# Kernel tuning notes

Measured on AMD Instinct MI355X. Metric: run time of the kernel, lower is better.

## Reference

```python
import jax, jax.numpy as jnp
import numpy as np

CUR, FULL, BS, DIM, H, D = 512, 1024, 4, 1024, 16, 64
PREV = FULL - CUR


def _rel_shift(x):
    # x: (cur, full, bs, h) -- TransformerXL relative shift (pad/reshape/slice)
    cur, full = x.shape[0], x.shape[1]
    zero_pad = jnp.zeros((cur, 1) + x.shape[2:], x.dtype)
    x_padded = jnp.concatenate([zero_pad, x], axis=1)           # (cur, full+1, bs, h)
    x_padded = x_padded.reshape((full + 1, cur) + x.shape[2:])  # view trick
    x = x_padded[1:].reshape(x.shape)
    tri = jnp.tril(jnp.ones((cur, full), x.dtype), full - cur)  # keep valid band
    return x * tri[:, :, None, None]


def setup_inputs() -> dict:
    key = jax.random.key(0)
    ks = jax.random.split(key, 12)
    s = jnp.float32(0.02)
    # causal mask: query i (at absolute pos i+PREV) may not attend to key j > i+PREV
    mask = (jnp.arange(FULL)[None, :] > (jnp.arange(CUR)[:, None] + PREV))[:, :, None]
    return {
        "inputs": jax.random.normal(ks[0], (CUR, BS, DIM), jnp.float32),
        "pos_embedding": jax.random.normal(ks[1], (FULL, 1, DIM), jnp.float32),
        "full_input": jax.random.normal(ks[2], (FULL, BS, DIM), jnp.float32),
        "u": jax.random.normal(ks[3], (H, D), jnp.float32) * s,
        "v": jax.random.normal(ks[4], (H, D), jnp.float32) * s,
        "W_kv": jax.random.normal(ks[5], (DIM, 2 * H * D), jnp.float32) * s,
        "b_kv": jnp.zeros((2 * H * D,), jnp.float32),
        "W_q": jax.random.normal(ks[6], (DIM, H * D), jnp.float32) * s,
        "b_q": jnp.zeros((H * D,), jnp.float32),
        "W_pos": jax.random.normal(ks[7], (DIM, H * D), jnp.float32) * s,
        "b_pos": jnp.zeros((H * D,), jnp.float32),
        "W_proj": jax.random.normal(ks[8], (H * D, DIM), jnp.float32) * s,
        "b_proj": jnp.zeros((DIM,), jnp.float32),
        "mask": mask,
    }


def reference(inputs, pos_embedding, full_input, u, v, W_kv, b_kv, W_q, b_q,
              W_pos, b_pos, W_proj, b_proj, mask):
    cur_seq, bs = inputs.shape[0], inputs.shape[1]
    full_seq = full_input.shape[0]
    scale = jnp.float32(1.0 / D ** 0.5)

    kv = full_input @ W_kv + b_kv                       # (full, bs, 2*H*D)
    key, value = jnp.split(kv, 2, axis=-1)
    query = inputs @ W_q + b_q                          # (cur, bs, H*D)
    r = (pos_embedding @ W_pos + b_pos).reshape(full_seq, H, D)

    key = key.reshape(full_seq, bs, H, D)
    value = value.reshape(full_seq, bs, H, D)
    query = query.reshape(cur_seq, bs, H, D)

    content_attn = jnp.einsum('ibhd,jbhd->ijbh', query + u, key)
    position_attn = jnp.einsum('ibhd,jhd->ijbh', query + v, r)
    position_attn = _rel_shift(position_attn)

    attn = (content_attn + position_attn) * scale       # (cur, full, bs, h)
    attn = jnp.where(mask[:, :, :, None], -jnp.inf, attn)
    attn = jax.nn.softmax(attn, axis=1)                 # softmax over full_seq

    attn_vec = jnp.einsum('ijbh,jbhd->ibhd', attn, value)
    attn_vec = attn_vec.reshape(cur_seq, bs, H * D)
    return attn_vec @ W_proj + b_proj                   # (cur, bs, DIM)
```

## Files before the change

### kernel.cpp

```cpp
#include <hip/hip_runtime.h>


typedef unsigned short u16;
typedef short short8 __attribute__((ext_vector_type(8)));
typedef float f32x4 __attribute__((ext_vector_type(4)));

#define BSZ 4
#define PREV 512

__device__ __forceinline__ float b2f(u16 u) {
  union { unsigned int i; float f; } x; x.i = ((unsigned int)u) << 16; return x.f;
}
__device__ __forceinline__ u16 f2b(float f) {
  union { float f; unsigned int i; } x; x.f = f;
  unsigned int u = x.i;
  return (u16)((u + 0x7fffu + ((u >> 16) & 1u)) >> 16);
}
__device__ __forceinline__ void storeC(u16* C, size_t idx, float v) { C[idx] = f2b(v); }
__device__ __forceinline__ void storeC(float* C, size_t idx, float v) { C[idx] = v; }

__device__ __forceinline__ void load_lds16(const u16* g, void* l) {
  __builtin_amdgcn_global_load_lds(
      (const __attribute__((address_space(1))) unsigned int*)g,
      (__attribute__((address_space(3))) unsigned int*)l, 16, 0, 0);
}

__device__ __forceinline__ size_t pidx8(int row, int k, int K32) {
  return (((size_t)((row >> 4) * K32 + (k >> 5))) << 9) +
         (((k >> 3) & 3) << 7) + ((row & 15) << 3);
}

__global__ __launch_bounds__(256)
void prep(const float* __restrict__ s0, const float* __restrict__ s1,
          const float* __restrict__ s2, u16* __restrict__ d0,
          u16* __restrict__ d1, u16* __restrict__ d2,
          const float* __restrict__ W0, const float* __restrict__ W1,
          const float* __restrict__ W2, const float* __restrict__ W3,
          u16* __restrict__ T0, u16* __restrict__ T1,
          u16* __restrict__ T2, u16* __restrict__ T3) {
  __shared__ u16 ld[64 * 66];
  const int bxg = blockIdx.x;
  if (bxg < 3584) {
    const float* s; u16* d; size_t base;
    if (bxg < 2048)      { s = s0; d = d0; base = (size_t)bxg * 2048; }
    else if (bxg < 3072) { s = s1; d = d1; base = (size_t)(bxg - 2048) * 2048; }
    else                 { s = s2; d = d2; base = (size_t)(bxg - 3072) * 2048; }
    size_t i = base + (size_t)threadIdx.x * 8;
    const f32x4* p = reinterpret_cast<const f32x4*>(s + i);
    f32x4 a = p[0], b = p[1];
    short8 r;
#pragma unroll
    for (int e = 0; e < 4; e++) { r[e] = (short)f2b(a[e]); r[e + 4] = (short)f2b(b[e]); }
    int row = (int)(i >> 10), k = (int)(i & 1023);
    *reinterpret_cast<short8*>(d + pidx8(row, k, 32)) = r;
    return;
  }
  const int l = bxg - 3584;
  const int z = l >> 9;
  const int rem = l & 511;
  const int bx = rem & 31, by = rem >> 5;
  const float* W; u16* T; int N;
  if (z == 0)      { W = W0; T = T0; N = 2048; }
  else if (z == 1) { W = W1; T = T1; N = 1024; }
  else if (z == 2) { W = W2; T = T2; N = 1024; }
  else             { W = W3; T = T3; N = 1024; }
  const int n0 = bx * 64, k0 = by * 64;
  if (n0 >= N) return;

  const int tid = threadIdx.x;
#pragma unroll
  for (int rep = 0; rep < 16; rep++) {
    int idx = tid + 256 * rep;
    int kk = idx >> 6, nn = idx & 63;
    ld[kk * 66 + nn] = f2b(W[(size_t)(k0 + kk) * N + n0 + nn]);
  }
  __syncthreads();
#pragma unroll
  for (int rep = 0; rep < 2; rep++) {
    int idx = tid + 256 * rep;
    int nn = idx >> 3, k8 = (idx & 7) * 8;
    short8 r;
#pragma unroll
    for (int e = 0; e < 8; e++) r[e] = (short)ld[(k8 + e) * 66 + nn];
    *reinterpret_cast<short8*>(T + pidx8(n0 + nn, k0 + k8, 32)) = r;
  }
}

template <typename OT, int MODE>
__device__ __forceinline__ void gemm_core(
    short* __restrict__ at, short* __restrict__ bt,
    const u16* __restrict__ A, const u16* __restrict__ BT,
    const float* __restrict__ bias, OT* __restrict__ C, u16* __restrict__ C2,
    int N, int K, int bx, int by)
{
  const int tid = threadIdx.x;
  const int lane = tid & 63, w = tid >> 6;
  const int wr = w >> 1, wc = w & 1;
  const int quad = lane >> 4, ml = lane & 15;
  const int row0 = by * 128, col0 = bx * 128;
  const int K32 = K >> 5;

  f32x4 acc[4][4];
  const f32x4 fzero = {0.f, 0.f, 0.f, 0.f};
#pragma unroll
  for (int i = 0; i < 4; i++)
#pragma unroll
    for (int j = 0; j < 4; j++) acc[i][j] = fzero;

  for (int k0 = 0; k0 < K; k0 += 64) {
    __syncthreads();
#pragma unroll
    for (int i = 0; i < 4; i++) {
      int c = 4 * w + i;
      int mc = c >> 1, kc = c & 1;
      size_t ca = ((size_t)(((row0 >> 4) + mc) * K32 + (k0 >> 5) + kc)) << 9;
      size_t cb = ((size_t)(((col0 >> 4) + mc) * K32 + (k0 >> 5) + kc)) << 9;
      load_lds16(A + ca + lane * 8, (void*)(at + c * 512));
      load_lds16(BT + cb + lane * 8, (void*)(bt + c * 512));
    }
    __syncthreads();

    short8 af[4][2], bf[4][2];
#pragma unroll
    for (int mc = 0; mc < 4; mc++)
#pragma unroll
      for (int kc = 0; kc < 2; kc++)
        af[mc][kc] = *reinterpret_cast<const short8*>(at + ((((wr * 4 + mc) * 2 + kc) * 64) + lane) * 8);
#pragma unroll
    for (int nc = 0; nc < 4; nc++)
#pragma unroll
      for (int kc = 0; kc < 2; kc++)
        bf[nc][kc] = *reinterpret_cast<const short8*>(bt + ((((wc * 4 + nc) * 2 + kc) * 64) + lane) * 8);

#pragma unroll
    for (int mc = 0; mc < 4; mc++)
#pragma unroll
      for (int nc = 0; nc < 4; nc++)
#pragma unroll
        for (int kc = 0; kc < 2; kc++)
          acc[mc][nc] = __builtin_amdgcn_mfma_f32_16x16x32_bf16(af[mc][kc], bf[nc][kc], acc[mc][nc], 0, 0, 0);
  }

#pragma unroll
  for (int nc = 0; nc < 4; nc++) {
    int col = col0 + wc * 64 + nc * 16 + ml;
    float bv = bias[col];
#pragma unroll
    for (int mc = 0; mc < 4; mc++) {
#pragma unroll
      for (int reg = 0; reg < 4; reg++) {
        int row = row0 + wr * 64 + mc * 16 + quad * 4 + reg;
        float val = acc[mc][nc][reg] + bv;
        if constexpr (MODE == 0) {
          storeC(C, (size_t)row * N + col, val);
        } else if constexpr (MODE == 1) {
          int j = row >> 2, bb = row & 3;
          int tile = j >> 6, jl = j & 63;
          if (col < 1024) {
            int h = col >> 6, d = col & 63;
            int ncj = jl >> 4, nlj = jl & 15, kcd = d >> 5, qdd = (d >> 3) & 3, jjd = d & 7;
            C[((size_t)(bb * 16 + h) * 16 + tile) * 4096 +
              ((ncj * 2 + kcd) * 64 + qdd * 16 + nlj) * 8 + jjd] = f2b(val);
          } else {
            int c2 = col - 1024;
            int h = c2 >> 6, d = c2 & 63;
            int ncd = d >> 4, nld = d & 15, kcj = jl >> 5, qdj = (jl >> 3) & 3, jjj = jl & 7;
            C2[((size_t)(bb * 16 + h) * 16 + tile) * 4096 +
               ((kcj * 4 + ncd) * 64 + qdj * 16 + nld) * 8 + jjj] = f2b(val);
          }
        } else {
          int h = col >> 6, d = col & 63;
          C[((size_t)h * 1024 + row) * 64 + d] = f2b(val);
        }
      }
    }
  }
}

__global__ __launch_bounds__(256, 2)
void gemm3(const u16* __restrict__ fibf, const u16* __restrict__ WkvT,
           const float* __restrict__ b_kv, u16* __restrict__ Kt2, u16* __restrict__ Vt2,
           const u16* __restrict__ inbf, const u16* __restrict__ WqT,
           const float* __restrict__ b_q, u16* __restrict__ qq,
           const u16* __restrict__ pebf, const u16* __restrict__ WposT,
           const float* __restrict__ b_pos, u16* __restrict__ Rt)
{
  __shared__ __align__(16) short at[8192];
  __shared__ __align__(16) short bt[8192];
  const int id = blockIdx.x;
  if (id < 512) {
    gemm_core<u16, 1>(at, bt, fibf, WkvT, b_kv, Kt2, Vt2, 2048, 1024, id & 15, id >> 4);
  } else if (id < 640) {
    const int l = id - 512;
    gemm_core<u16, 0>(at, bt, inbf, WqT, b_q, qq, (u16*)nullptr, 1024, 1024, l & 7, l >> 3);
  } else {
    const int l = id - 640;
    gemm_core<u16, 2>(at, bt, pebf, WposT, b_pos, Rt, (u16*)nullptr, 1024, 1024, l & 7, l >> 3);
  }
}

__global__ __launch_bounds__(256, 2)
void gemm_proj(const u16* __restrict__ A, const u16* __restrict__ BT,
               const float* __restrict__ bias, float* __restrict__ C)
{
  __shared__ __align__(16) short at[8192];
  __shared__ __align__(16) short bt[8192];
  gemm_core<float, 0>(at, bt, A, BT, bias, C, (u16*)nullptr, 1024, 1024,
                      blockIdx.x, blockIdx.y);
}

__global__ __launch_bounds__(256, 4)
void flash_xl(const u16* __restrict__ q, const u16* __restrict__ Kt2,
              const u16* __restrict__ Vt2, const u16* __restrict__ Rt,
              const float* __restrict__ u, const float* __restrict__ v,
              float* __restrict__ po, float* __restrict__ pm,
              float* __restrict__ pl)
{
  __shared__ __align__(16) short kb[4096];
  __shared__ __align__(16) short vb[4096];
  __shared__ __align__(16) short pt[4][1024];

  const int tid = threadIdx.x, lane = tid & 63, w = tid >> 6;
  const int quad = lane >> 4, ml = lane & 15;
  const int x = blockIdx.x;
  const int it = 7 - (x >> 1), s = x & 1;
  const int nt = it + 9;
  const int nt0 = (nt + 1) >> 1;
  const int ts = s ? nt0 : 0, te = s ? nt : nt0;

  const int b = blockIdx.y, h = blockIdx.z;
  const int bh = b * 16 + h;
  const int i0 = it * 64, ig0 = i0 + w * 16;

  const u16* Kbase = Kt2 + ((size_t)(b * 16 + h) * 16) * 4096;
  const u16* Vbase = Vt2 + ((size_t)(b * 16 + h) * 16) * 4096;
  const u16* Rp = Rt + (size_t)h * 65536;

  short8 qu[2], qvf[2];
  {
    int ig = ig0 + ml;
#pragma unroll
    for (int kc = 0; kc < 2; kc++) {
      int dbase = kc * 32 + quad * 8;
      short8 qq = *reinterpret_cast<const short8*>(q + ((size_t)ig * BSZ + b) * 1024 + h * 64 + dbase);
      const f32x4* up = reinterpret_cast<const f32x4*>(u + h * 64 + dbase);
      const f32x4* vp = reinterpret_cast<const f32x4*>(v + h * 64 + dbase);
      f32x4 u0 = up[0], u1 = up[1], v0 = vp[0], v1 = vp[1];
#pragma unroll
      for (int e = 0; e < 8; e++) {
        float qf = b2f((u16)qq[e]);
        float uu = (e < 4) ? u0[e] : u1[e - 4];
        float vv = (e < 4) ? v0[e] : v1[e - 4];
        qu[kc][e]  = (short)f2b((qf + uu) * 0.125f);
        qvf[kc][e] = (short)f2b((qf + vv) * 0.125f);
      }
    }
  }

  short8 kones;
#pragma unroll
  for (int e = 0; e < 8; e++) kones[e] = (short)0x3F80;

  const f32x4 fzero = {0.f, 0.f, 0.f, 0.f};
  f32x4 o_acc[4];
#pragma unroll
  for (int i = 0; i < 4; i++) o_acc[i] = fzero;
  float m_run[4], l_run[4];
#pragma unroll
  for (int i = 0; i < 4; i++) { m_run[i] = -1e30f; l_run[i] = 0.f; }

  short8 pk0, pk1, pv0, pv1;
  {
    const u16* kg = Kbase + (size_t)ts * 4096;
    const u16* vg = Vbase + (size_t)ts * 4096;
    pk0 = *reinterpret_cast<const short8*>(kg + tid * 8);
    pk1 = *reinterpret_cast<const short8*>(kg + 2048 + tid * 8);
    pv0 = *reinterpret_cast<const short8*>(vg + tid * 8);
    pv1 = *reinterpret_cast<const short8*>(vg + 2048 + tid * 8);
  }

  for (int t = ts; t < te; t++) {
    const int j0 = t * 64;
    __syncthreads();
    *reinterpret_cast<short8*>(kb + tid * 8) = pk0;
    *reinterpret_cast<short8*>(kb + 2048 + tid * 8) = pk1;
    *reinterpret_cast<short8*>(vb + tid * 8) = pv0;
    *reinterpret_cast<short8*>(vb + 2048 + tid * 8) = pv1;
    __syncthreads();

    if (t + 1 < te) {
      const u16* kg = Kbase + (size_t)(t + 1) * 4096;
      const u16* vg = Vbase + (size_t)(t + 1) * 4096;
      pk0 = *reinterpret_cast<const short8*>(kg + tid * 8);
      pk1 = *reinterpret_cast<const short8*>(kg + 2048 + tid * 8);
      pv0 = *reinterpret_cast<const short8*>(vg + tid * 8);
      pv1 = *reinterpret_cast<const short8*>(vg + 2048 + tid * 8);
    }

    f32x4 sc[4];
#pragma unroll
    for (int nc = 0; nc < 4; nc++) {
      sc[nc] = fzero;
#pragma unroll
      for (int kc = 0; kc < 2; kc++) {
        short8 kf = *reinterpret_cast<const short8*>(kb + ((nc * 2 + kc) * 64 + lane) * 8);
        sc[nc] = __builtin_amdgcn_mfma_f32_16x16x32_bf16(qu[kc], kf, sc[nc], 0, 0, 0);
      }
    }
    const int relstart = j0 - ig0 + 496;
    f32x4 p2[5];
#pragma unroll
    for (int c = 0; c < 5; c++) {
      p2[c] = fzero;
      int rel = relstart + c * 16 + ml;
      if (rel > 1023) rel = 1023;
      const u16* rp = Rp + (size_t)rel * 64 + quad * 8;
#pragma unroll
      for (int kc = 0; kc < 2; kc++) {
        short8 rf = *reinterpret_cast<const short8*>(rp + kc * 32);
        p2[c] = __builtin_amdgcn_mfma_f32_16x16x32_bf16(qvf[kc], rf, p2[c], 0, 0, 0);
      }
    }

    const bool anymask = (j0 + 63) > (ig0 + PREV);
    float pv_[4][4];
    float tmax[4] = {-1e30f, -1e30f, -1e30f, -1e30f};
#pragma unroll
    for (int reg = 0; reg < 4; reg++) {
      int rowl = quad * 4 + reg;
      int src = quad * 16 + ((ml - rowl - 1) & 15);
      bool hi = ml > rowl;
      float sh[5];
#pragma unroll
      for (int c = 0; c < 5; c++) sh[c] = __shfl(p2[c][reg], src, 64);
#pragma unroll
      for (int nc = 0; nc < 4; nc++) {
        float sv = sc[nc][reg] + (hi ? sh[nc + 1] : sh[nc]);
        if (anymask) {
          int jg = j0 + nc * 16 + ml;
          if (jg > ig0 + rowl + PREV) sv = -1e30f;
        }
        pv_[nc][reg] = sv;
        tmax[reg] = fmaxf(tmax[reg], sv);
      }
    }
#pragma unroll
    for (int reg = 0; reg < 4; reg++) {
      float tm = tmax[reg];
#pragma unroll
      for (int off = 1; off < 16; off <<= 1) tm = fmaxf(tm, __shfl_xor(tm, off, 64));
      float mnew = fmaxf(m_run[reg], tm);
      float alpha = __expf(m_run[reg] - mnew);
#pragma unroll
      for (int nc = 0; nc < 4; nc++)
        pv_[nc][reg] = __expf(pv_[nc][reg] - mnew);
      l_run[reg] *= alpha;
      m_run[reg] = mnew;
#pragma unroll
      for (int nc = 0; nc < 4; nc++) o_acc[nc][reg] *= alpha;
    }

#pragma unroll
    for (int nc = 0; nc < 4; nc++) {
      int jl = nc * 16 + ml;
      int kc = nc >> 1, qdj = (jl >> 3) & 3, jj = ml & 7;
#pragma unroll
      for (int reg = 0; reg < 4; reg++) {
        int rowl = quad * 4 + reg;
        pt[w][(kc * 64 + qdj * 16 + rowl) * 8 + jj] = (short)f2b(pv_[nc][reg]);
      }
    }
    short8 pf[2];
    pf[0] = *reinterpret_cast<const short8*>(pt[w] + (0 * 64 + lane) * 8);
    pf[1] = *reinterpret_cast<const short8*>(pt[w] + (1 * 64 + lane) * 8);

    f32x4 lsum = fzero;
    lsum = __builtin_amdgcn_mfma_f32_16x16x32_bf16(pf[0], kones, lsum, 0, 0, 0);
    lsum = __builtin_amdgcn_mfma_f32_16x16x32_bf16(pf[1], kones, lsum, 0, 0, 0);

#pragma unroll
    for (int ncd = 0; ncd < 4; ncd++)
#pragma unroll
      for (int kc = 0; kc < 2; kc++) {
        short8 vf = *reinterpret_cast<const short8*>(vb + ((kc * 4 + ncd) * 64 + lane) * 8);
        o_acc[ncd] = __builtin_amdgcn_mfma_f32_16x16x32_bf16(pf[kc], vf, o_acc[ncd], 0, 0, 0);
      }
#pragma unroll
    for (int reg = 0; reg < 4; reg++) l_run[reg] += lsum[reg];
  }

#pragma unroll
  for (int reg = 0; reg < 4; reg++) {
    int ig = ig0 + quad * 4 + reg;
    size_t ridx = (size_t)(s * 512 + ig) * 64 + bh;
    if (ml == 0) { pm[ridx] = m_run[reg]; pl[ridx] = l_run[reg]; }
#pragma unroll
    for (int ncd = 0; ncd < 4; ncd++)
      po[ridx * 64 + ncd * 16 + ml] = o_acc[ncd][reg];
  }
}

__global__ __launch_bounds__(256)
void combine(const float* __restrict__ po, const float* __restrict__ pm,
             const float* __restrict__ pl, u16* __restrict__ av) {
  int t = blockIdx.x * 256 + threadIdx.x;
  int r0 = t >> 3, d8 = (t & 7) * 8;
  int ig = r0 >> 6, b = (r0 >> 4) & 3, h = r0 & 15;
  float m1 = pm[r0], m2 = pm[32768 + r0];
  float l1 = pl[r0], l2 = pl[32768 + r0];
  const f32x4* p1 = reinterpret_cast<const f32x4*>(po + (size_t)r0 * 64 + d8);
  const f32x4* p2 = reinterpret_cast<const f32x4*>(po + ((size_t)32768 + r0) * 64 + d8);
  f32x4 o1a = p1[0], o1b = p1[1], o2a = p2[0], o2b = p2[1];
  float m = fmaxf(m1, m2);
  float a1 = __expf(m1 - m), a2 = __expf(m2 - m);
  float l = l1 * a1 + l2 * a2;
  short8 r;
#pragma unroll
  for (int e = 0; e < 4; e++) {
    r[e]     = (short)f2b((o1a[e] * a1 + o2a[e] * a2) / l);
    r[e + 4] = (short)f2b((o1b[e] * a1 + o2b[e] * a2) / l);
  }
  int row = ig * 4 + b, k = h * 64 + d8;
  *reinterpret_cast<short8*>(av + pidx8(row, k, 32)) = r;
}

extern "C" void kernel_launch(void* const* d_in, const int* in_sizes, int n_in,
                              void* d_out, int out_size, void* d_ws, size_t ws_size,
                              hipStream_t stream) {
  (void)in_sizes; (void)n_in; (void)out_size; (void)ws_size;

  const float* inputs  = (const float*)d_in[0];
  const float* pos_emb = (const float*)d_in[1];
  const float* full_in = (const float*)d_in[2];
  const float* u       = (const float*)d_in[3];
  const float* v       = (const float*)d_in[4];
  const float* W_kv    = (const float*)d_in[5];
  const float* b_kv    = (const float*)d_in[6];
  const float* W_q     = (const float*)d_in[7];
  const float* b_q     = (const float*)d_in[8];
  const float* W_pos   = (const float*)d_in[9];
  const float* b_pos   = (const float*)d_in[10];
  const float* W_proj  = (const float*)d_in[11];
  const float* b_proj  = (const float*)d_in[12];
  float* out = (float*)d_out;

  char* ws = (char*)d_ws;
  u16* Kt2   = (u16*)(ws);
  u16* Vt2   = (u16*)(ws + ( 8u << 20));
  u16* qq    = (u16*)(ws + (16u << 20));
  u16* Rt    = (u16*)(ws + (20u << 20));
  u16* av    = (u16*)(ws + (22u << 20));
  u16* WkvT  = (u16*)(ws + (26u << 20));
  u16* WqT   = (u16*)(ws + (30u << 20));
  u16* WposT = (u16*)(ws + (32u << 20));
  u16* WprojT= (u16*)(ws + (34u << 20));
  u16* fibf  = (u16*)(ws + (36u << 20));
  u16* inbf  = (u16*)(ws + (44u << 20));
  u16* pebf  = (u16*)(ws + (48u << 20));
  float* po  = (float*)(ws + (36u << 20));
  float* pm  = (float*)(ws + (52u << 20));
  float* pl  = (float*)(ws + (52u << 20) + (256u << 10));

  hipLaunchKernelGGL(prep, dim3(5632), dim3(256), 0, stream,
                     full_in, inputs, pos_emb, fibf, inbf, pebf,
                     W_kv, W_q, W_pos, W_proj, WkvT, WqT, WposT, WprojT);

  hipLaunchKernelGGL(gemm3, dim3(704), dim3(256), 0, stream,
                     fibf, WkvT, b_kv, Kt2, Vt2,
                     inbf, WqT, b_q, qq,
                     pebf, WposT, b_pos, Rt);

  hipLaunchKernelGGL(flash_xl, dim3(16, 4, 16), dim3(256), 0, stream,
                     qq, Kt2, Vt2, Rt, u, v, po, pm, pl);
  hipLaunchKernelGGL(combine, dim3(1024), dim3(256), 0, stream, po, pm, pl, av);

  hipLaunchKernelGGL(gemm_proj, dim3(8, 16), dim3(256), 0, stream,
                     av, WprojT, b_proj, out);
}
```

Baseline: 223.1 us.

## Fuse split-KV combine into flash kernel via atomic last-arriver merge

```diff
diff --git a/kernel.cpp b/kernel.cpp
--- a/kernel.cpp
+++ b/kernel.cpp
@@ -31,21 +31,21 @@
 }
 
 __global__ __launch_bounds__(256)
-void prep(const float* __restrict__ s0, const float* __restrict__ s1,
-          const float* __restrict__ s2, u16* __restrict__ d0,
-          u16* __restrict__ d1, u16* __restrict__ d2,
-          const float* __restrict__ W0, const float* __restrict__ W1,
-          const float* __restrict__ W2, const float* __restrict__ W3,
-          u16* __restrict__ T0, u16* __restrict__ T1,
-          u16* __restrict__ T2, u16* __restrict__ T3) {
+void prep_k(const float* __restrict__ s0, const float* __restrict__ s1,
+            const float* __restrict__ s2, u16* __restrict__ d0,
+            u16* __restrict__ d1, u16* __restrict__ d2,
+            const float* __restrict__ W0, const float* __restrict__ W1,
+            const float* __restrict__ W2, const float* __restrict__ W3,
+            u16* __restrict__ T0, u16* __restrict__ T1,
+            u16* __restrict__ T2, u16* __restrict__ T3) {
   __shared__ u16 ld[64 * 66];
-  const int bxg = blockIdx.x;
+  const int bxg = blockIdx.x, tid = threadIdx.x;
   if (bxg < 3584) {
     const float* s; u16* d; size_t base;
     if (bxg < 2048)      { s = s0; d = d0; base = (size_t)bxg * 2048; }
     else if (bxg < 3072) { s = s1; d = d1; base = (size_t)(bxg - 2048) * 2048; }
     else                 { s = s2; d = d2; base = (size_t)(bxg - 3072) * 2048; }
-    size_t i = base + (size_t)threadIdx.x * 8;
+    size_t i = base + (size_t)tid * 8;
     const f32x4* p = reinterpret_cast<const f32x4*>(s + i);
     f32x4 a = p[0], b = p[1];
     short8 r;
@@ -67,7 +67,6 @@
   const int n0 = bx * 64, k0 = by * 64;
   if (n0 >= N) return;
 
-  const int tid = threadIdx.x;
 #pragma unroll
   for (int rep = 0; rep < 16; rep++) {
     int idx = tid + 256 * rep;
@@ -178,12 +177,12 @@
 }
 
 __global__ __launch_bounds__(256, 2)
-void gemm3(const u16* __restrict__ fibf, const u16* __restrict__ WkvT,
-           const float* __restrict__ b_kv, u16* __restrict__ Kt2, u16* __restrict__ Vt2,
-           const u16* __restrict__ inbf, const u16* __restrict__ WqT,
-           const float* __restrict__ b_q, u16* __restrict__ qq,
-           const u16* __restrict__ pebf, const u16* __restrict__ WposT,
-           const float* __restrict__ b_pos, u16* __restrict__ Rt)
+void gemm3_k(const u16* __restrict__ fibf, const u16* __restrict__ WkvT,
+             const float* __restrict__ b_kv, u16* __restrict__ Kt2, u16* __restrict__ Vt2,
+             const u16* __restrict__ inbf, const u16* __restrict__ WqT,
+             const float* __restrict__ b_q, u16* __restrict__ qq,
+             const u16* __restrict__ pebf, const u16* __restrict__ WposT,
+             const float* __restrict__ b_pos, u16* __restrict__ Rt)
 {
   __shared__ __align__(16) short at[8192];
   __shared__ __align__(16) short bt[8192];
@@ -200,8 +199,8 @@
 }
 
 __global__ __launch_bounds__(256, 2)
-void gemm_proj(const u16* __restrict__ A, const u16* __restrict__ BT,
-               const float* __restrict__ bias, float* __restrict__ C)
+void gemm_proj_k(const u16* __restrict__ A, const u16* __restrict__ BT,
+                 const float* __restrict__ bias, float* __restrict__ C)
 {
   __shared__ __align__(16) short at[8192];
   __shared__ __align__(16) short bt[8192];
@@ -210,17 +209,20 @@
 }
 
 __global__ __launch_bounds__(256, 4)
-void flash_xl(const u16* __restrict__ q, const u16* __restrict__ Kt2,
-              const u16* __restrict__ Vt2, const u16* __restrict__ Rt,
-              const float* __restrict__ u, const float* __restrict__ v,
-              float* __restrict__ po, float* __restrict__ pm,
-              float* __restrict__ pl)
+void flash_k(const u16* __restrict__ q, const u16* __restrict__ Kt2,
+             const u16* __restrict__ Vt2, const u16* __restrict__ Rt,
+             const float* __restrict__ u, const float* __restrict__ v,
+             float* __restrict__ po, float* __restrict__ pm,
+             float* __restrict__ pl, u16* __restrict__ av,
+             unsigned* __restrict__ flags)
 {
   __shared__ __align__(16) short kb[4096];
   __shared__ __align__(16) short vb[4096];
   __shared__ __align__(16) short pt[4][1024];
+  __shared__ unsigned sec;
 
   const int tid = threadIdx.x, lane = tid & 63, w = tid >> 6;
+  short* ptw = pt[w];
   const int quad = lane >> 4, ml = lane & 15;
   const int x = blockIdx.x;
   const int it = 7 - (x >> 1), s = x & 1;
@@ -367,12 +369,12 @@
 #pragma unroll
       for (int reg = 0; reg < 4; reg++) {
         int rowl = quad * 4 + reg;
-        pt[w][(kc * 64 + qdj * 16 + rowl) * 8 + jj] = (short)f2b(pv_[nc][reg]);
+        ptw[(kc * 64 + qdj * 16 + rowl) * 8 + jj] = (short)f2b(pv_[nc][reg]);
       }
     }
     short8 pf[2];
-    pf[0] = *reinterpret_cast<const short8*>(pt[w] + (0 * 64 + lane) * 8);
-    pf[1] = *reinterpret_cast<const short8*>(pt[w] + (1 * 64 + lane) * 8);
+    pf[0] = *reinterpret_cast<const short8*>(ptw + (0 * 64 + lane) * 8);
+    pf[1] = *reinterpret_cast<const short8*>(ptw + (1 * 64 + lane) * 8);
 
     f32x4 lsum = fzero;
     lsum = __builtin_amdgcn_mfma_f32_16x16x32_bf16(pf[0], kones, lsum, 0, 0, 0);
@@ -398,30 +400,37 @@
     for (int ncd = 0; ncd < 4; ncd++)
       po[ridx * 64 + ncd * 16 + ml] = o_acc[ncd][reg];
   }
-}
-
-__global__ __launch_bounds__(256)
-void combine(const float* __restrict__ po, const float* __restrict__ pm,
-             const float* __restrict__ pl, u16* __restrict__ av) {
-  int t = blockIdx.x * 256 + threadIdx.x;
-  int r0 = t >> 3, d8 = (t & 7) * 8;
-  int ig = r0 >> 6, b = (r0 >> 4) & 3, h = r0 & 15;
-  float m1 = pm[r0], m2 = pm[32768 + r0];
-  float l1 = pl[r0], l2 = pl[32768 + r0];
-  const f32x4* p1 = reinterpret_cast<const f32x4*>(po + (size_t)r0 * 64 + d8);
-  const f32x4* p2 = reinterpret_cast<const f32x4*>(po + ((size_t)32768 + r0) * 64 + d8);
-  f32x4 o1a = p1[0], o1b = p1[1], o2a = p2[0], o2b = p2[1];
-  float m = fmaxf(m1, m2);
-  float a1 = __expf(m1 - m), a2 = __expf(m2 - m);
-  float l = l1 * a1 + l2 * a2;
-  short8 r;
-#pragma unroll
-  for (int e = 0; e < 4; e++) {
-    r[e]     = (short)f2b((o1a[e] * a1 + o2a[e] * a2) / l);
-    r[e + 4] = (short)f2b((o1b[e] * a1 + o2b[e] * a2) / l);
-  }
-  int row = ig * 4 + b, k = h * 64 + d8;
-  *reinterpret_cast<short8*>(av + pidx8(row, k, 32)) = r;
+
+  __syncthreads();
+  __threadfence();
+  if (tid == 0) {
+    unsigned old = __hip_atomic_fetch_add(flags + ((x >> 1) * 64 + bh), 1u,
+                                          __ATOMIC_ACQ_REL, __HIP_MEMORY_SCOPE_AGENT);
+    sec = old;
+  }
+  __syncthreads();
+  if (sec) {
+    __threadfence();
+#pragma unroll
+    for (int reg = 0; reg < 4; reg++) {
+      int ig = ig0 + quad * 4 + reg;
+      size_t prid = (size_t)((s ^ 1) * 512 + ig) * 64 + bh;
+      float m2 = pm[prid], l2 = pl[prid];
+      float m1 = m_run[reg], l1 = l_run[reg];
+      float m = fmaxf(m1, m2);
+      float a1 = __expf(m1 - m), a2 = __expf(m2 - m);
+      float linv = 1.f / (l1 * a1 + l2 * a2);
+      int row = ig * 4 + b;
+#pragma unroll
+      for (int ncd = 0; ncd < 4; ncd++) {
+        int d = ncd * 16 + ml;
+        float o2 = po[prid * 64 + d];
+        float val = (o_acc[ncd][reg] * a1 + o2 * a2) * linv;
+        int k = h * 64 + d;
+        av[pidx8(row, k, 32) + (k & 7)] = f2b(val);
+      }
+    }
+  }
 }
 
 extern "C" void kernel_launch(void* const* d_in, const int* in_sizes, int n_in,
@@ -443,8 +452,8 @@
   const float* W_proj  = (const float*)d_in[11];
   const float* b_proj  = (const float*)d_in[12];
   float* out = (float*)d_out;
-
   char* ws = (char*)d_ws;
+
   u16* Kt2   = (u16*)(ws);
   u16* Vt2   = (u16*)(ws + ( 8u << 20));
   u16* qq    = (u16*)(ws + (16u << 20));
@@ -460,20 +469,22 @@
   float* po  = (float*)(ws + (36u << 20));
   float* pm  = (float*)(ws + (52u << 20));
   float* pl  = (float*)(ws + (52u << 20) + (256u << 10));
-
-  hipLaunchKernelGGL(prep, dim3(5632), dim3(256), 0, stream,
+  unsigned* flags = (unsigned*)(ws + (56u << 20));
+
+  hipMemsetAsync(flags, 0, 512 * sizeof(unsigned), stream);
+
+  hipLaunchKernelGGL(prep_k, dim3(5632), dim3(256), 0, stream,
                      full_in, inputs, pos_emb, fibf, inbf, pebf,
                      W_kv, W_q, W_pos, W_proj, WkvT, WqT, WposT, WprojT);
 
-  hipLaunchKernelGGL(gemm3, dim3(704), dim3(256), 0, stream,
+  hipLaunchKernelGGL(gemm3_k, dim3(704), dim3(256), 0, stream,
                      fibf, WkvT, b_kv, Kt2, Vt2,
                      inbf, WqT, b_q, qq,
                      pebf, WposT, b_pos, Rt);
 
-  hipLaunchKernelGGL(flash_xl, dim3(16, 4, 16), dim3(256), 0, stream,
-                     qq, Kt2, Vt2, Rt, u, v, po, pm, pl);
-  hipLaunchKernelGGL(combine, dim3(1024), dim3(256), 0, stream, po, pm, pl, av);
-
-  hipLaunchKernelGGL(gemm_proj, dim3(8, 16), dim3(256), 0, stream,
+  hipLaunchKernelGGL(flash_k, dim3(16, 4, 16), dim3(256), 0, stream,
+                     qq, Kt2, Vt2, Rt, u, v, po, pm, pl, av, flags);
+
+  hipLaunchKernelGGL(gemm_proj_k, dim3(8, 16), dim3(256), 0, stream,
                      av, WprojT, b_proj, out);
 }
```

Result: slower. 490.6 us (+119.9%).
